# Kernel optimization log

Measured on AMD Instinct MI355X. Metric: run time of the kernel, lower is better.

Reference implementation:

```python
import jax, jax.numpy as jnp
import numpy as np

NUM_ROUTES = 8
TEMPERATURE = 0.1
NEG_INF = -1e9
EPS = 1e-12  # F.normalize eps


def _l2_normalize(t):
    n = jnp.sqrt(jnp.sum(t * t, axis=-1, keepdims=True))
    return t / jnp.maximum(n, EPS)


def setup_inputs() -> dict:
    key = jax.random.key(0)
    ks = jax.random.split(key, 7)
    B, P1, D = 4, 2049, 1024
    s = 1.0 / np.sqrt(D)
    return {
        "x": jax.random.normal(ks[0], (B, P1, D), jnp.float32),
        "Wq": jax.random.normal(ks[1], (D, D), jnp.float32) * s,
        "bq": jax.random.normal(ks[2], (D,), jnp.float32) * 0.01,
        "Wk": jax.random.normal(ks[3], (D, D), jnp.float32) * s,
        "bk": jax.random.normal(ks[4], (D,), jnp.float32) * 0.01,
        "Wv": jax.random.normal(ks[5], (D, D), jnp.float32) * s,
        "bv": jax.random.normal(ks[6], (D,), jnp.float32) * 0.01,
    }


def reference(x, Wq, bq, Wk, bk, Wv, bv):
    x = x[:, 1:, :]  # skip_first=True
    B, P, D = x.shape
    q = _l2_normalize(x @ Wq.T + bq)
    k = _l2_normalize(x @ Wk.T + bk)
    v = x @ Wv.T + bv
    scores = jnp.einsum('bpd,bqd->bpq', q, k)  # [B,P,P]
    diag = jnp.eye(P, dtype=bool)
    scores = jnp.where(diag[None], NEG_INF, scores)
    topk_scores, routes = jax.lax.top_k(scores / TEMPERATURE, NUM_ROUTES)  # [B,P,K]
    weights = jax.nn.softmax(topk_scores, axis=-1)
    b_idx = jnp.arange(B)[:, None, None]
    v_gathered = v[b_idx, routes]  # [B,P,K,D]
    features = jnp.einsum('bpk,bpkd->bpd', weights, v_gathered)
    return routes, weights, features
```

## Files before the change

kernel.cpp:

```cpp
#include <hip/hip_runtime.h>
#include <hip/hip_bf16.h>
#include <math.h>

#define TEMP 0.1
#define NC 10

typedef float f4 __attribute__((ext_vector_type(4)));
typedef short s8v __attribute__((ext_vector_type(8)));
typedef int   i4v __attribute__((ext_vector_type(4)));
typedef _Float16 h8v __attribute__((ext_vector_type(8)));

__device__ inline short f2bf(float f) {
    __hip_bfloat16 h = __float2bfloat16(f);
    return *reinterpret_cast<short*>(&h);
}

__device__ __forceinline__ void g2l16(const void* g, void* l) {
    __builtin_amdgcn_global_load_lds(
        (const __attribute__((address_space(1))) void*)g,
        (__attribute__((address_space(3))) void*)l, 16, 0, 0);
}

__global__ __launch_bounds__(256) void prep_w(
    const float* __restrict__ Wq, const float* __restrict__ Wk,
    const float* __restrict__ Wv,
    signed char* __restrict__ Wql, signed char* __restrict__ Wkl,
    double* __restrict__ wqsc, double* __restrict__ wksc,
    short* __restrict__ Wvh)
{
    const int row = blockIdx.x, tid = threadIdx.x;
    const int which = blockIdx.y;
    if (which == 2) {
        const float4 v = ((const float4*)(Wv + (size_t)row * 1024))[tid];
        __align__(8) short h[4] = {f2bf(v.x), f2bf(v.y), f2bf(v.z), f2bf(v.w)};
        *(short4*)&Wvh[(size_t)row * 1024 + tid * 4] = *(short4*)h;
        return;
    }
    const float* src = which ? Wk : Wq;
    signed char* limbs = which ? Wkl : Wql;
    double* scale = which ? wksc : wqsc;
    const long plane_stride = 1024L * 1024;

    const float4 v = ((const float4*)(src + (size_t)row * 1024))[tid];
    float m = fmaxf(fmaxf(fabsf(v.x), fabsf(v.y)), fmaxf(fabsf(v.z), fabsf(v.w)));
#pragma unroll
    for (int off = 32; off > 0; off >>= 1) m = fmaxf(m, __shfl_down(m, off));
    __shared__ float wmax[4];
    __shared__ int ssig;
    if ((tid & 63) == 0) wmax[tid >> 6] = m;
    __syncthreads();
    if (tid == 0) {
        float rm = fmaxf(fmaxf(wmax[0], wmax[1]), fmaxf(wmax[2], wmax[3]));
        int sig = (rm > 0.f) ? (29 - ilogbf(rm)) : 0;
        ssig = sig;
        scale[row] = ldexp(1.0, -sig);
    }
    __syncthreads();
    const double s2 = ldexp(1.0, ssig);
    float xs[4] = {v.x, v.y, v.z, v.w};
    signed char out[4][4];
#pragma unroll
    for (int e = 0; e < 4; ++e) {
        long X = __double2ll_rn((double)xs[e] * s2);
#pragma unroll
        for (int l = 0; l < 3; ++l) {
            int d = (int)(((X + 128) & 255) - 128);
            out[l][e] = (signed char)d;
            X = (X - d) >> 8;
        }
        out[3][e] = (signed char)X;
    }
#pragma unroll
    for (int l = 0; l < 4; ++l)
        *(char4*)&limbs[(size_t)l * plane_stride + (size_t)row * 1024 + tid * 4] =
            *(char4*)&out[l][0];
}

__global__ __launch_bounds__(256) void prep_x(
    const float* __restrict__ src, signed char* __restrict__ limbs,
    long plane_stride, double* __restrict__ scale,
    short* __restrict__ hi)
{
    const int row = blockIdx.x, tid = threadIdx.x;
    const float4 v = ((const float4*)(src + (size_t)row * 1024))[tid];
    float m = fmaxf(fmaxf(fabsf(v.x), fabsf(v.y)), fmaxf(fabsf(v.z), fabsf(v.w)));
#pragma unroll
    for (int off = 32; off > 0; off >>= 1) m = fmaxf(m, __shfl_down(m, off));
    __shared__ float wmax[4];
    __shared__ int ssig;
    if ((tid & 63) == 0) wmax[tid >> 6] = m;
    __syncthreads();
    if (tid == 0) {
        float rm = fmaxf(fmaxf(wmax[0], wmax[1]), fmaxf(wmax[2], wmax[3]));
        int sig = (rm > 0.f) ? (29 - ilogbf(rm)) : 0;
        ssig = sig;
        scale[row] = ldexp(1.0, -sig);
    }
    __syncthreads();
    const double s2 = ldexp(1.0, ssig);
    float xs[4] = {v.x, v.y, v.z, v.w};
    signed char out[4][4];
    __align__(8) short h[4];
#pragma unroll
    for (int e = 0; e < 4; ++e) {
        long X = __double2ll_rn((double)xs[e] * s2);
#pragma unroll
        for (int lmb = 0; lmb < 3; ++lmb) {
            int d = (int)(((X + 128) & 255) - 128);
            out[lmb][e] = (signed char)d;
            X = (X - d) >> 8;
        }
        out[3][e] = (signed char)X;
        h[e] = f2bf(xs[e]);
    }
#pragma unroll
    for (int lmb = 0; lmb < 4; ++lmb)
        *(char4*)&limbs[(size_t)lmb * plane_stride + (size_t)row * 1024 + tid * 4] =
            *(char4*)&out[lmb][0];
    *(short4*)&hi[(size_t)row * 1024 + tid * 4] = *(short4*)h;
}

__global__ __launch_bounds__(256, 4) void gemm_i8qk(
    const signed char* __restrict__ Xl,
    const signed char* __restrict__ Wql,
    const signed char* __restrict__ Wkl,
    const double* __restrict__ xsc,
    const double* __restrict__ wqsc, const double* __restrict__ wksc,
    const float* __restrict__ bq, const float* __restrict__ bk,
    float* __restrict__ Qf, float* __restrict__ Kf)
{
    const int K = 1024, N = 1024;
    const long MK = 2048L * 1024, NK = 1024L * 1024;
    const signed char* Wl = blockIdx.z ? Wkl : Wql;
    const double* wsc = blockIdx.z ? wksc : wqsc;
    const float* bias = blockIdx.z ? bk : bq;
    float* C = blockIdx.z ? Kf : Qf;

    __shared__ __align__(16) signed char Asm[4][64][64];
    __shared__ __align__(16) signed char Bsm[4][64][64];

    const int tid  = threadIdx.x;
    const int lane = tid & 63, wave = tid >> 6;
    const int wm = wave >> 1, wn = wave & 1;
    const int quad = lane >> 4, l16 = lane & 15;
    const int m0 = blockIdx.y * 64, n0 = blockIdx.x * 64;

    const int srow = tid >> 2;
    const int cswz = ((tid & 3) ^ ((srow >> 1) & 3));
    const signed char* ap = Xl + (size_t)(m0 + srow) * K + cswz * 16;
    const signed char* bp = Wl + (size_t)(n0 + srow) * K + cswz * 16;

    signed char* aw = (signed char*)Asm + (wave << 10);
    signed char* bw = (signed char*)Bsm + (wave << 10);

    i4v acc[4][2][2] = {};

    for (int k0 = 0; k0 < K; k0 += 64) {
        __syncthreads();
#pragma unroll
        for (int l = 0; l < 4; ++l) {
            g2l16(ap + l * MK + k0, aw + l * 4096);
            g2l16(bp + l * NK + k0, bw + l * 4096);
        }
        __syncthreads();

        i4v bF[4][2];
#pragma unroll
        for (int j = 0; j < 4; ++j)
#pragma unroll
            for (int nt = 0; nt < 2; ++nt) {
                const int R = wn * 32 + nt * 16 + l16;
                bF[j][nt] = *(const i4v*)&Bsm[j][R][(quad ^ ((R >> 1) & 3)) * 16];
            }

#pragma unroll
        for (int i = 0; i < 4; ++i) {
            const int R0 = wm * 32 + l16;
            const int R1 = wm * 32 + 16 + l16;
            i4v a0 = *(const i4v*)&Asm[i][R0][(quad ^ ((R0 >> 1) & 3)) * 16];
            i4v a1 = *(const i4v*)&Asm[i][R1][(quad ^ ((R1 >> 1) & 3)) * 16];
#pragma unroll
            for (int j = 0; j < 4; ++j) {
                if (i + j < 3) continue;
                const int s = i + j - 3;
                acc[s][0][0] = __builtin_amdgcn_mfma_i32_16x16x64_i8(a0, bF[j][0], acc[s][0][0], 0, 0, 0);
                acc[s][0][1] = __builtin_amdgcn_mfma_i32_16x16x64_i8(a0, bF[j][1], acc[s][0][1], 0, 0, 0);
                acc[s][1][0] = __builtin_amdgcn_mfma_i32_16x16x64_i8(a1, bF[j][0], acc[s][1][0], 0, 0, 0);
                acc[s][1][1] = __builtin_amdgcn_mfma_i32_16x16x64_i8(a1, bF[j][1], acc[s][1][1], 0, 0, 0);
            }
        }
    }

    const double wt0 = ldexp(1.0, 24), wt1 = ldexp(1.0, 32);
    const double wt2 = ldexp(1.0, 40), wt3 = ldexp(1.0, 48);
#pragma unroll
    for (int mt = 0; mt < 2; ++mt)
#pragma unroll
        for (int nt = 0; nt < 2; ++nt)
#pragma unroll
            for (int r = 0; r < 4; ++r) {
                int row = m0 + wm * 32 + mt * 16 + quad * 4 + r;
                int col = n0 + wn * 32 + nt * 16 + l16;
                double dsum = wt0 * (double)acc[0][mt][nt][r]
                            + wt1 * (double)acc[1][mt][nt][r]
                            + wt2 * (double)acc[2][mt][nt][r]
                            + wt3 * (double)acc[3][mt][nt][r];
                C[(size_t)row * N + col] =
                    (float)(dsum * xsc[row] * wsc[col] + (double)bias[col]);
            }
}

__global__ __launch_bounds__(256, 4) void gemm_v64(
    const short* __restrict__ Ahp, const short* __restrict__ Bhp,
    const float* __restrict__ bias, float* __restrict__ C)
{
    const int K = 1024, N = 1024;
    __shared__ __align__(16) short Ah[64][32];
    __shared__ __align__(16) short Bh[64][32];

    const int tid = threadIdx.x, lane = tid & 63, wave = tid >> 6;
    const int wm = wave >> 1, wn = wave & 1;
    const int quad = lane >> 4, l16 = lane & 15;
    const int m0 = blockIdx.y * 64, n0 = blockIdx.x * 64;
    const int srow = tid >> 2;
    const int cswz = ((tid & 3) ^ ((srow >> 1) & 3));
    const char* ap = (const char*)(Ahp + (size_t)(m0 + srow) * K) + cswz * 16;
    const char* bp = (const char*)(Bhp + (size_t)(n0 + srow) * K) + cswz * 16;
    char* aw = (char*)Ah + (wave << 10);
    char* bw = (char*)Bh + (wave << 10);

    f4 acc[2][2] = {};
    for (int k0 = 0; k0 < K; k0 += 32) {
        __syncthreads();
        g2l16(ap + 2 * k0, aw);
        g2l16(bp + 2 * k0, bw);
        __syncthreads();

        s8v af[2], bf[2];
#pragma unroll
        for (int t = 0; t < 2; ++t) {
            const int Ra = wm * 32 + t * 16 + l16;
            const int Rb = wn * 32 + t * 16 + l16;
            af[t] = *(const s8v*)((const char*)Ah + Ra * 64 + ((quad ^ ((Ra >> 1) & 3)) << 4));
            bf[t] = *(const s8v*)((const char*)Bh + Rb * 64 + ((quad ^ ((Rb >> 1) & 3)) << 4));
        }
#pragma unroll
        for (int mt = 0; mt < 2; ++mt)
#pragma unroll
            for (int nt = 0; nt < 2; ++nt)
                acc[mt][nt] = __builtin_amdgcn_mfma_f32_16x16x32_bf16(
                    af[mt], bf[nt], acc[mt][nt], 0, 0, 0);
    }
#pragma unroll
    for (int mt = 0; mt < 2; ++mt)
#pragma unroll
        for (int nt = 0; nt < 2; ++nt)
#pragma unroll
            for (int r = 0; r < 4; ++r) {
                int row = m0 + wm * 32 + mt * 16 + quad * 4 + r;
                int col = n0 + wn * 32 + nt * 16 + l16;
                C[(size_t)row * N + col] = acc[mt][nt][r] + bias[col];
            }
}

__global__ __launch_bounds__(256, 4) void gemm_score(
    const short* __restrict__ Qh, const short* __restrict__ Kh,
    float* __restrict__ C)
{
    const int K = 1024, N = 2048;
    __shared__ __align__(16) short As[64][32];
    __shared__ __align__(16) short Bs[64][32];
    const int tid = threadIdx.x, lane = tid & 63, wave = tid >> 6;
    const int wm = wave >> 1, wn = wave & 1;
    const int quad = lane >> 4, l16 = lane & 15;
    const int m0 = blockIdx.y * 64, n0 = blockIdx.x * 64;
    const int srow = tid >> 2;
    const int cswz = ((tid & 3) ^ ((srow >> 1) & 3));
    const char* ap = (const char*)(Qh + (size_t)(m0 + srow) * K) + cswz * 16;
    const char* bp = (const char*)(Kh + (size_t)(n0 + srow) * K) + cswz * 16;
    char* aw = (char*)As + (wave << 10);
    char* bw = (char*)Bs + (wave << 10);

    f4 acc[2][2] = {};
    for (int k0 = 0; k0 < K; k0 += 32) {
        __syncthreads();
        g2l16(ap + 2 * k0, aw);
        g2l16(bp + 2 * k0, bw);
        __syncthreads();

        h8v af[2], bf[2];
#pragma unroll
        for (int t = 0; t < 2; ++t) {
            const int Ra = wm * 32 + t * 16 + l16;
            const int Rb = wn * 32 + t * 16 + l16;
            af[t] = *(const h8v*)((const char*)As + Ra * 64 + ((quad ^ ((Ra >> 1) & 3)) << 4));
            bf[t] = *(const h8v*)((const char*)Bs + Rb * 64 + ((quad ^ ((Rb >> 1) & 3)) << 4));
        }
#pragma unroll
        for (int mt = 0; mt < 2; ++mt)
#pragma unroll
            for (int nt = 0; nt < 2; ++nt)
                acc[mt][nt] = __builtin_amdgcn_mfma_f32_16x16x32_f16(
                    af[mt], bf[nt], acc[mt][nt], 0, 0, 0);
    }
#pragma unroll
    for (int mt = 0; mt < 2; ++mt)
#pragma unroll
        for (int nt = 0; nt < 2; ++nt)
#pragma unroll
            for (int r = 0; r < 4; ++r) {
                int row = m0 + wm * 32 + mt * 16 + quad * 4 + r;
                int col = n0 + wn * 32 + nt * 16 + l16;
                C[(size_t)row * N + col] = acc[mt][nt][r];
            }
}

__global__ __launch_bounds__(256) void l2norm_f32h16(
    float* __restrict__ fq, float* __restrict__ fk,
    short* __restrict__ hq, short* __restrict__ hk)
{
    float* f = blockIdx.y ? fk : fq;
    short* h = blockIdx.y ? hk : hq;
    const int row = blockIdx.x;
    const int tid = threadIdx.x;
    float4* p4 = (float4*)(f + (size_t)row * 1024);
    float4 v = p4[tid];
    double s = (double)v.x * v.x + (double)v.y * v.y
             + (double)v.z * v.z + (double)v.w * v.w;
#pragma unroll
    for (int off = 32; off > 0; off >>= 1) s += __shfl_down(s, off);
    __shared__ double ws[5];
    if ((tid & 63) == 0) ws[tid >> 6] = s;
    __syncthreads();
    if (tid == 0) ws[4] = fmax(sqrt(ws[0] + ws[1] + ws[2] + ws[3]), 1e-12);
    __syncthreads();
    const double inv = 1.0 / ws[4];
    float o0 = (float)(v.x * inv), o1 = (float)(v.y * inv);
    float o2 = (float)(v.z * inv), o3 = (float)(v.w * inv);
    float4 o = make_float4(o0, o1, o2, o3);
    p4[tid] = o;
    __align__(8) _Float16 hv[4] = {(_Float16)o0, (_Float16)o1,
                                   (_Float16)o2, (_Float16)o3};
    *(short4*)&h[(size_t)row * 1024 + tid * 4] = *(short4*)hv;
}

__global__ __launch_bounds__(256) void topk_route(
    const float*  __restrict__ S,
    const float*  __restrict__ Qf,
    const float*  __restrict__ Kf,
    const float*  __restrict__ Vf,
    float* __restrict__ routes_out,
    float* __restrict__ weights_out,
    float* __restrict__ feat_out,
    int batch)
{
    const int P = 2048, D = 1024;
    __shared__ float  qrow[1024];
    __shared__ float  cval[4 * NC];
    __shared__ int    cidx[4 * NC];
    __shared__ int    sel[NC];
    __shared__ double cscore[NC];
    __shared__ int    topi_s[8];
    __shared__ float  wts[8];

    const int p = blockIdx.x;
    const int tid = threadIdx.x;
    const int lane = tid & 63, wave = tid >> 6;

    const float4* sr4 = (const float4*)(S + (size_t)p * P);
    const float4 s0 = sr4[tid];
    const float4 s1 = sr4[tid + 256];
    ((float4*)qrow)[tid] = ((const float4*)(Qf + (size_t)p * D))[tid];

    float v[8] = {s0.x, s0.y, s0.z, s0.w, s1.x, s1.y, s1.z, s1.w};
    int   ji[8];
#pragma unroll
    for (int e = 0; e < 8; ++e) {
        ji[e] = (e < 4) ? (4 * tid + e) : (1024 + 4 * tid + (e - 4));
        if (ji[e] == p) v[e] = -1e30f;
    }

    float lv = v[0]; int li = ji[0];
#pragma unroll
    for (int e = 1; e < 8; ++e)
        if (v[e] > lv) { lv = v[e]; li = ji[e]; }

    float cv_ = -INFINITY; int ci_ = 0x7fffffff;
#pragma unroll 1
    for (int it = 0; it < NC; ++it) {
        float bv = lv; int bi = li;
#pragma unroll
        for (int off = 32; off > 0; off >>= 1) {
            float ov = __shfl_xor(bv, off);
            int   oi = __shfl_xor(bi, off);
            if (ov > bv || (ov == bv && oi < bi)) { bv = ov; bi = oi; }
        }
        if (lane == it) { cv_ = bv; ci_ = bi; }
#pragma unroll
        for (int e = 0; e < 8; ++e)
            if (ji[e] == bi) v[e] = -INFINITY;
        lv = v[0]; li = ji[0];
#pragma unroll
        for (int e = 1; e < 8; ++e)
            if (v[e] > lv) { lv = v[e]; li = ji[e]; }
    }
    if (lane < NC) { cval[wave * NC + lane] = cv_; cidx[wave * NC + lane] = ci_; }
    __syncthreads();

    if (wave == 0) {
        float mv = (lane < 4 * NC) ? cval[lane] : -INFINITY;
        int   mi = (lane < 4 * NC) ? cidx[lane] : 0x7fffffff;
        int rank = 0;
#pragma unroll 1
        for (int j = 0; j < 4 * NC; ++j) {
            float vj = __shfl(mv, j);
            int   ij = __shfl(mi, j);
            rank += (vj > mv || (vj == mv && ij < mi)) ? 1 : 0;
        }
        if (lane < 4 * NC && rank < NC) sel[rank] = mi;
    }
    __syncthreads();

    float pfv[8];
#pragma unroll
    for (int c = 0; c < 8; ++c)
        pfv[c] = Vf[(size_t)sel[c] * D + tid * 4];

    {
        const float* k0r = Kf + (size_t)sel[wave] * D;
        const float* k1r = Kf + (size_t)sel[wave + 4] * D;
        const float* k2r = Kf + (size_t)sel[8 + (wave & 1)] * D;
        double a0 = 0.0, a1 = 0.0, a2 = 0.0;
#pragma unroll 4
        for (int j = 0; j < 8; ++j) {
            const int e = lane * 2 + j * 128;
            const float2 q2 = *(const float2*)&qrow[e];
            const float2 kA = *(const float2*)&k0r[e];
            const float2 kB = *(const float2*)&k1r[e];
            const float2 kC = *(const float2*)&k2r[e];
            a0 = fma((double)q2.x, (double)kA.x, fma((double)q2.y, (double)kA.y, a0));
            a1 = fma((double)q2.x, (double)kB.x, fma((double)q2.y, (double)kB.y, a1));
            a2 = fma((double)q2.x, (double)kC.x, fma((double)q2.y, (double)kC.y, a2));
        }
#pragma unroll
        for (int off = 32; off > 0; off >>= 1) {
            a0 += __shfl_xor(a0, off);
            a1 += __shfl_xor(a1, off);
            a2 += __shfl_xor(a2, off);
        }
        if (lane == 0) {
            cscore[wave]     = a0;
            cscore[wave + 4] = a1;
            if (wave < 2) cscore[8 + wave] = a2;
        }
    }

    {
        float pf = 0.f;
#pragma unroll
        for (int c = 0; c < 8; ++c) pf += pfv[c];
        asm volatile("" :: "v"(pf));
    }
    __syncthreads();

    if (wave == 0) {
        double sc_ = (lane < NC) ? cscore[lane] : -1.0e308;
        int    id_ = (lane < NC) ? sel[lane]    : 0x7fffffff;
        int rank = 0;
#pragma unroll
        for (int j = 0; j < NC; ++j) {
            double vj = __shfl(sc_, j);
            int    ij = __shfl(id_, j);
            rank += (vj > sc_ || (vj == sc_ && ij < id_)) ? 1 : 0;
        }
        double mm = sc_;
#pragma unroll
        for (int off = 32; off > 0; off >>= 1) mm = fmax(mm, __shfl_xor(mm, off));
        double e = (rank < 8 && lane < NC) ? exp((sc_ - mm) / TEMP) : 0.0;
        double sum = e;
#pragma unroll
        for (int off = 32; off > 0; off >>= 1) sum += __shfl_xor(sum, off);
        if (rank < 8 && lane < NC) {
            float wk = (float)(e / sum);
            wts[rank] = wk; topi_s[rank] = id_;
            const size_t row = (size_t)batch * P + p;
            routes_out[row * 8 + rank]  = (float)id_;
            weights_out[row * 8 + rank] = wk;
        }
    }
    __syncthreads();

    float4 a = {0.f, 0.f, 0.f, 0.f};
#pragma unroll
    for (int k = 0; k < 8; ++k) {
        const float4 v4 = ((const float4*)(Vf + (size_t)topi_s[k] * D))[tid];
        float wk = wts[k];
        a.x = fmaf(wk, v4.x, a.x);
        a.y = fmaf(wk, v4.y, a.y);
        a.z = fmaf(wk, v4.z, a.z);
        a.w = fmaf(wk, v4.w, a.w);
    }
    ((float4*)(feat_out + ((size_t)batch * P + p) * D))[tid] = a;
}

extern "C" void kernel_launch(void* const* d_in, const int* in_sizes, int n_in,
                              void* d_out, int out_size, void* d_ws, size_t ws_size,
                              hipStream_t stream)
{
    const float* x  = (const float*)d_in[0];
    const float* Wq = (const float*)d_in[1];
    const float* bq = (const float*)d_in[2];
    const float* Wk = (const float*)d_in[3];
    const float* bk = (const float*)d_in[4];
    const float* Wv = (const float*)d_in[5];
    const float* bv = (const float*)d_in[6];

    const int B = 4, P = 2048, D = 1024;
    const size_t PD = (size_t)P * D;
    const size_t DD = (size_t)D * D;

    float*  Qf   = (float*)d_ws;
    float*  Kf   = Qf + PD;
    double* xsc  = (double*)(Kf + PD);
    double* wqsc = xsc + 2048;
    double* wksc = wqsc + 1024;
    short*  Qh   = (short*)(wksc + 1024);
    short*  Kh   = Qh + PD;
    short*  xh   = Kh + PD;
    short*  Wvh  = xh + PD;
    float*  Vf   = (float*)(Wvh + DD);
    float*  Sf   = Vf + PD;
    signed char* Xl  = (signed char*)(Sf + (size_t)P * P);
    signed char* Wql = Xl + 4 * PD;
    signed char* Wkl = Wql + 4 * DD;

    float* out     = (float*)d_out;
    float* routes  = out;
    float* weights = out + (size_t)B * P * 8;
    float* feat    = out + (size_t)B * P * 16;

    dim3 blk(256);
    prep_w<<<dim3(1024, 3), blk, 0, stream>>>(Wq, Wk, Wv, Wql, Wkl, wqsc, wksc, Wvh);

    for (int b = 0; b < B; ++b) {
        const float* xb = x + ((size_t)b * 2049 + 1) * D;
        prep_x<<<dim3(P), blk, 0, stream>>>(xb, Xl, (long)PD, xsc, xh);
        gemm_i8qk<<<dim3(16, 32, 2), blk, 0, stream>>>(Xl, Wql, Wkl, xsc, wqsc, wksc,
                                                       bq, bk, Qf, Kf);
        gemm_v64<<<dim3(16, 32), blk, 0, stream>>>(xh, Wvh, bv, Vf);
        l2norm_f32h16<<<dim3(P, 2), blk, 0, stream>>>(Qf, Kf, Qh, Kh);
        gemm_score<<<dim3(32, 32), blk, 0, stream>>>(Qh, Kh, Sf);
        topk_route<<<dim3(P), blk, 0, stream>>>(Sf, Qf, Kf, Vf, routes, weights, feat, b);
    }
}
```

Baseline: 629.4 us.

## Load GEMM operands directly to registers and prefetch all candidate V rows

The int8 QK GEMM now loads its A operand straight from global memory into registers, prefetching the next K slice, instead of staging it through LDS. The bf16 V GEMM and the fp16 score GEMM drop LDS and both barriers entirely, reading MFMA fragments from global memory per wave, and lose their occupancy hint in launch bounds. The top-k kernel now loads all 10 candidate V rows as float4 before scoring and accumulates features with zero weights for the non-selected candidates, removing the dependent second gather. This trades LDS traffic and syncs for uncoalesced global reads, more register pressure, and lower L2 reuse.

```diff
diff --git a/kernel.cpp b/kernel.cpp
--- a/kernel.cpp
+++ b/kernel.cpp
@@ -136,7 +136,6 @@
     const float* bias = blockIdx.z ? bk : bq;
     float* C = blockIdx.z ? Kf : Qf;
 
-    __shared__ __align__(16) signed char Asm[4][64][64];
     __shared__ __align__(16) signed char Bsm[4][64][64];
 
     const int tid  = threadIdx.x;
@@ -147,21 +146,26 @@
 
     const int srow = tid >> 2;
     const int cswz = ((tid & 3) ^ ((srow >> 1) & 3));
-    const signed char* ap = Xl + (size_t)(m0 + srow) * K + cswz * 16;
     const signed char* bp = Wl + (size_t)(n0 + srow) * K + cswz * 16;
-
-    signed char* aw = (signed char*)Asm + (wave << 10);
     signed char* bw = (signed char*)Bsm + (wave << 10);
 
+    const signed char* a0p = Xl + (size_t)(m0 + wm * 32 + l16) * K + quad * 16;
+    const signed char* a1p = a0p + 16 * K;
+
     i4v acc[4][2][2] = {};
+
+    i4v at0[4], at1[4];
+#pragma unroll
+    for (int i = 0; i < 4; ++i) {
+        at0[i] = *(const i4v*)(a0p + i * MK);
+        at1[i] = *(const i4v*)(a1p + i * MK);
+    }
 
     for (int k0 = 0; k0 < K; k0 += 64) {
         __syncthreads();
 #pragma unroll
-        for (int l = 0; l < 4; ++l) {
-            g2l16(ap + l * MK + k0, aw + l * 4096);
+        for (int l = 0; l < 4; ++l)
             g2l16(bp + l * NK + k0, bw + l * 4096);
-        }
         __syncthreads();
 
         i4v bF[4][2];
@@ -175,10 +179,7 @@
 
 #pragma unroll
         for (int i = 0; i < 4; ++i) {
-            const int R0 = wm * 32 + l16;
-            const int R1 = wm * 32 + 16 + l16;
-            i4v a0 = *(const i4v*)&Asm[i][R0][(quad ^ ((R0 >> 1) & 3)) * 16];
-            i4v a1 = *(const i4v*)&Asm[i][R1][(quad ^ ((R1 >> 1) & 3)) * 16];
+            i4v a0 = at0[i], a1 = at1[i];
 #pragma unroll
             for (int j = 0; j < 4; ++j) {
                 if (i + j < 3) continue;
@@ -187,6 +188,14 @@
                 acc[s][0][1] = __builtin_amdgcn_mfma_i32_16x16x64_i8(a0, bF[j][1], acc[s][0][1], 0, 0, 0);
                 acc[s][1][0] = __builtin_amdgcn_mfma_i32_16x16x64_i8(a1, bF[j][0], acc[s][1][0], 0, 0, 0);
                 acc[s][1][1] = __builtin_amdgcn_mfma_i32_16x16x64_i8(a1, bF[j][1], acc[s][1][1], 0, 0, 0);
+            }
+        }
+
+        if (k0 + 64 < K) {
+#pragma unroll
+            for (int i = 0; i < 4; ++i) {
+                at0[i] = *(const i4v*)(a0p + i * MK + k0 + 64);
+                at1[i] = *(const i4v*)(a1p + i * MK + k0 + 64);
             }
         }
     }
@@ -210,39 +219,26 @@
             }
 }
 
-__global__ __launch_bounds__(256, 4) void gemm_v64(
+__global__ __launch_bounds__(256) void gemm_v64(
     const short* __restrict__ Ahp, const short* __restrict__ Bhp,
     const float* __restrict__ bias, float* __restrict__ C)
 {
     const int K = 1024, N = 1024;
-    __shared__ __align__(16) short Ah[64][32];
-    __shared__ __align__(16) short Bh[64][32];
-
     const int tid = threadIdx.x, lane = tid & 63, wave = tid >> 6;
     const int wm = wave >> 1, wn = wave & 1;
     const int quad = lane >> 4, l16 = lane & 15;
     const int m0 = blockIdx.y * 64, n0 = blockIdx.x * 64;
-    const int srow = tid >> 2;
-    const int cswz = ((tid & 3) ^ ((srow >> 1) & 3));
-    const char* ap = (const char*)(Ahp + (size_t)(m0 + srow) * K) + cswz * 16;
-    const char* bp = (const char*)(Bhp + (size_t)(n0 + srow) * K) + cswz * 16;
-    char* aw = (char*)Ah + (wave << 10);
-    char* bw = (char*)Bh + (wave << 10);
+
+    const short* aq = Ahp + (size_t)(m0 + wm * 32 + l16) * K + quad * 8;
+    const short* bqp = Bhp + (size_t)(n0 + wn * 32 + l16) * K + quad * 8;
 
     f4 acc[2][2] = {};
     for (int k0 = 0; k0 < K; k0 += 32) {
-        __syncthreads();
-        g2l16(ap + 2 * k0, aw);
-        g2l16(bp + 2 * k0, bw);
-        __syncthreads();
-
         s8v af[2], bf[2];
 #pragma unroll
         for (int t = 0; t < 2; ++t) {
-            const int Ra = wm * 32 + t * 16 + l16;
-            const int Rb = wn * 32 + t * 16 + l16;
-            af[t] = *(const s8v*)((const char*)Ah + Ra * 64 + ((quad ^ ((Ra >> 1) & 3)) << 4));
-            bf[t] = *(const s8v*)((const char*)Bh + Rb * 64 + ((quad ^ ((Rb >> 1) & 3)) << 4));
+            af[t] = *(const s8v*)(aq  + (size_t)t * 16 * K + k0);
+            bf[t] = *(const s8v*)(bqp + (size_t)t * 16 * K + k0);
         }
 #pragma unroll
         for (int mt = 0; mt < 2; ++mt)
@@ -263,38 +259,26 @@
             }
 }
 
-__global__ __launch_bounds__(256, 4) void gemm_score(
+__global__ __launch_bounds__(256) void gemm_score(
     const short* __restrict__ Qh, const short* __restrict__ Kh,
     float* __restrict__ C)
 {
     const int K = 1024, N = 2048;
-    __shared__ __align__(16) short As[64][32];
-    __shared__ __align__(16) short Bs[64][32];
     const int tid = threadIdx.x, lane = tid & 63, wave = tid >> 6;
     const int wm = wave >> 1, wn = wave & 1;
     const int quad = lane >> 4, l16 = lane & 15;
     const int m0 = blockIdx.y * 64, n0 = blockIdx.x * 64;
-    const int srow = tid >> 2;
-    const int cswz = ((tid & 3) ^ ((srow >> 1) & 3));
-    const char* ap = (const char*)(Qh + (size_t)(m0 + srow) * K) + cswz * 16;
-    const char* bp = (const char*)(Kh + (size_t)(n0 + srow) * K) + cswz * 16;
-    char* aw = (char*)As + (wave << 10);
-    char* bw = (char*)Bs + (wave << 10);
+
+    const short* aq = Qh + (size_t)(m0 + wm * 32 + l16) * K + quad * 8;
+    const short* bqp = Kh + (size_t)(n0 + wn * 32 + l16) * K + quad * 8;
 
     f4 acc[2][2] = {};
     for (int k0 = 0; k0 < K; k0 += 32) {
-        __syncthreads();
-        g2l16(ap + 2 * k0, aw);
-        g2l16(bp + 2 * k0, bw);
-        __syncthreads();
-
         h8v af[2], bf[2];
 #pragma unroll
         for (int t = 0; t < 2; ++t) {
-            const int Ra = wm * 32 + t * 16 + l16;
-            const int Rb = wn * 32 + t * 16 + l16;
-            af[t] = *(const h8v*)((const char*)As + Ra * 64 + ((quad ^ ((Ra >> 1) & 3)) << 4));
-            bf[t] = *(const h8v*)((const char*)Bs + Rb * 64 + ((quad ^ ((Rb >> 1) & 3)) << 4));
+            af[t] = *(const h8v*)(aq  + (size_t)t * 16 * K + k0);
+            bf[t] = *(const h8v*)(bqp + (size_t)t * 16 * K + k0);
         }
 #pragma unroll
         for (int mt = 0; mt < 2; ++mt)
@@ -360,8 +344,7 @@
     __shared__ int    cidx[4 * NC];
     __shared__ int    sel[NC];
     __shared__ double cscore[NC];
-    __shared__ int    topi_s[8];
-    __shared__ float  wts[8];
+    __shared__ float  wsel[NC];
 
     const int p = blockIdx.x;
     const int tid = threadIdx.x;
@@ -421,10 +404,10 @@
     }
     __syncthreads();
 
-    float pfv[8];
-#pragma unroll
-    for (int c = 0; c < 8; ++c)
-        pfv[c] = Vf[(size_t)sel[c] * D + tid * 4];
+    float4 pfv4[NC];
+#pragma unroll
+    for (int c = 0; c < NC; ++c)
+        pfv4[c] = ((const float4*)(Vf + (size_t)sel[c] * D))[tid];
 
     {
         const float* k0r = Kf + (size_t)sel[wave] * D;
@@ -454,13 +437,6 @@
             if (wave < 2) cscore[8 + wave] = a2;
         }
     }
-
-    {
-        float pf = 0.f;
-#pragma unroll
-        for (int c = 0; c < 8; ++c) pf += pfv[c];
-        asm volatile("" :: "v"(pf));
-    }
     __syncthreads();
 
     if (wave == 0) {
@@ -480,25 +456,26 @@
         double sum = e;
 #pragma unroll
         for (int off = 32; off > 0; off >>= 1) sum += __shfl_xor(sum, off);
-        if (rank < 8 && lane < NC) {
+        if (lane < NC) {
             float wk = (float)(e / sum);
-            wts[rank] = wk; topi_s[rank] = id_;
-            const size_t row = (size_t)batch * P + p;
-            routes_out[row * 8 + rank]  = (float)id_;
-            weights_out[row * 8 + rank] = wk;
+            wsel[lane] = wk;
+            if (rank < 8) {
+                const size_t row = (size_t)batch * P + p;
+                routes_out[row * 8 + rank]  = (float)id_;
+                weights_out[row * 8 + rank] = wk;
+            }
         }
     }
     __syncthreads();
 
     float4 a = {0.f, 0.f, 0.f, 0.f};
 #pragma unroll
-    for (int k = 0; k < 8; ++k) {
-        const float4 v4 = ((const float4*)(Vf + (size_t)topi_s[k] * D))[tid];
-        float wk = wts[k];
-        a.x = fmaf(wk, v4.x, a.x);
-        a.y = fmaf(wk, v4.y, a.y);
-        a.z = fmaf(wk, v4.z, a.z);
-        a.w = fmaf(wk, v4.w, a.w);
+    for (int c = 0; c < NC; ++c) {
+        const float wk = wsel[c];
+        a.x = fmaf(wk, pfv4[c].x, a.x);
+        a.y = fmaf(wk, pfv4[c].y, a.y);
+        a.z = fmaf(wk, pfv4[c].z, a.z);
+        a.w = fmaf(wk, pfv4[c].w, a.w);
     }
     ((float4*)(feat_out + ((size_t)batch * P + p) * D))[tid] = a;
 }
```

After: 969.2 us. 1.54x slower.
